# Kernel tuning notes

Measured on AMD Instinct MI355X. Metric: run time of the kernel, lower is better.

## Reference

```python
import jax, jax.numpy as jnp
import numpy as np

HID = 1024
NH = 16
HD = HID // NH  # 64


def _lin_params(key, fan_in, fan_out):
    k1, k2 = jax.random.split(key)
    lim = 1.0 / np.sqrt(fan_in)
    W = jax.random.uniform(k1, (fan_in, fan_out), jnp.float32, -lim, lim)
    b = jax.random.uniform(k2, (fan_out,), jnp.float32, -lim, lim)
    return W, b


def setup_inputs() -> dict:
    key = jax.random.key(0)
    ks = jax.random.split(key, 12)
    B, S = 4, 1024
    inp = {
        'query': jax.random.normal(ks[0], (B, S, HID), jnp.float32),
        'key': jax.random.normal(ks[1], (B, S, HID), jnp.float32),
        'value': jax.random.normal(ks[2], (B, S, HID), jnp.float32),
    }
    inp['Wq'], inp['bq'] = _lin_params(ks[3], HID, HID)
    inp['Wk'], inp['bk'] = _lin_params(ks[4], HID, HID)
    inp['Wv'], inp['bv'] = _lin_params(ks[5], HID, HID)
    inp['Wp'], inp['bp'] = _lin_params(ks[6], HID, HID)
    inp['Wup'], inp['bup'] = _lin_params(ks[7], HD, 1)
    inp['Wud'], inp['bud'] = _lin_params(ks[8], HD, 1)
    inp['Wus'], inp['bus'] = _lin_params(ks[9], HID, NH)
    inp['Wo'], inp['bo'] = _lin_params(ks[10], HID, HID)
    return inp


def _split_heads(x, B, S):
    # [B,S,HID] -> [B,NH,S,HD]
    return x.reshape(B, S, NH, HD).transpose(0, 2, 1, 3)


def reference(query, key, value, Wq, bq, Wk, bk, Wv, bv, Wp, bp,
              Wup, bup, Wud, bud, Wus, bus, Wo, bo):
    B, S, _ = query.shape
    len_q = S

    q = query @ Wq + bq   # [B,S,HID]
    k = key @ Wk + bk
    v = value @ Wv + bv

    # Gaussian-window positional bias (per head, per query position)
    p = _split_heads(q @ Wp + bp, B, S)              # [B,NH,S,HD]
    tp = jnp.tanh(p)
    p_i = tp @ Wup + bup                             # [B,NH,S,1]
    z_i = tp @ Wud + bud                             # [B,NH,S,1]
    cen_pos = len_q * jax.nn.sigmoid(p_i)            # [B,NH,S,1]
    win_size = len_q * jax.nn.sigmoid(z_i)           # [B,NH,S,1]
    pos = jnp.arange(len_q, dtype=q.dtype)[None, None, None, :]  # [1,1,1,S]
    bias = (pos - cen_pos) ** 2 / (0.5 * win_size ** 2)          # [B,NH,S,S]

    # per-head alpha gate from raw query
    alpha = jax.nn.sigmoid(query @ Wus + bus)        # [B,S,NH]
    alpha = alpha.reshape(B, S, NH, 1).transpose(0, 2, 1, 3)  # [B,NH,S,1]

    qh = _split_heads(q, B, S)
    kh = _split_heads(k, B, S)
    vh = _split_heads(v, B, S)

    scale = 1.0 / jnp.sqrt(jnp.asarray(HD, q.dtype))
    scores = jnp.einsum('bhqd,bhkd->bhqk', qh, kh) * scale
    scores = scores - alpha * bias                   # inject gated Gaussian bias
    attn = jax.nn.softmax(scores, axis=-1)           # [B,NH,S,S]

    out = jnp.einsum('bhqk,bhkd->bhqd', attn, vh)    # [B,NH,S,HD]
    x = out.transpose(0, 2, 1, 3).reshape(B, S, HID)
    x = x @ Wo + bo
    return x, attn
```

## Files before the change

### kernel.cpp

```cpp
#include <hip/hip_runtime.h>
#include <hip/hip_bf16.h>
#include <math.h>

#define S_LEN 1024
#define HIDN  1024
#define NHEAD 16
#define HDIM  64
#define BATCH 4
#define MTOT  (BATCH * S_LEN)

typedef __attribute__((ext_vector_type(8))) short          bf16v8;
typedef __attribute__((ext_vector_type(8))) unsigned short u16v8;
typedef __attribute__((ext_vector_type(4))) unsigned short u16v4;
typedef __attribute__((ext_vector_type(4))) float          f32v4;

__device__ __forceinline__ unsigned short f2bf_rne(float x) {
    unsigned int u = __float_as_uint(x);
    unsigned int r = (u + 0x7fffu + ((u >> 16) & 1u)) >> 16;
    return (unsigned short)r;
}
__device__ __forceinline__ float bf2f(unsigned short h) {
    return __uint_as_float(((unsigned int)h) << 16);
}
__device__ __forceinline__ void split2(float x, unsigned short& h, unsigned short& l) {
    h = f2bf_rne(x);
    l = f2bf_rne(x - bf2f(h));
}

__global__ __launch_bounds__(256) void split_a(
    const float* __restrict__ X, unsigned short* __restrict__ H,
    unsigned short* __restrict__ L)
{
    const int i = blockIdx.x * 256 + threadIdx.x;
    const float4 x0 = ((const float4*)X)[2 * i];
    const float4 x1 = ((const float4*)X)[2 * i + 1];
    float xs[8] = {x0.x, x0.y, x0.z, x0.w, x1.x, x1.y, x1.z, x1.w};
    u16v8 h, l;
#pragma unroll
    for (int j = 0; j < 8; ++j) {
        unsigned short hh, ll;
        split2(xs[j], hh, ll);
        h[j] = hh; l[j] = ll;
    }
    ((u16v8*)H)[i] = h;
    ((u16v8*)L)[i] = l;
}

__global__ __launch_bounds__(256) void split_w(
    const float* __restrict__ W, unsigned short* __restrict__ H,
    unsigned short* __restrict__ L)
{
    __shared__ float T[64][65];
    const int t  = threadIdx.x;
    const int k0 = blockIdx.y * 64;
    const int n0 = blockIdx.x * 64;

    const int r = t >> 4;
    const int c = (t & 15) * 4;
#pragma unroll
    for (int i = 0; i < 4; ++i) {
        const int rr = r + i * 16;
        const float4 v = *(const float4*)&W[(size_t)(k0 + rr) * 1024 + n0 + c];
        T[rr][c + 0] = v.x; T[rr][c + 1] = v.y;
        T[rr][c + 2] = v.z; T[rr][c + 3] = v.w;
    }
    __syncthreads();

    const int n  = t >> 2;
    const int ko = (t & 3) * 16;
    u16v8 h0, h1, l0, l1;
#pragma unroll
    for (int kk = 0; kk < 8; ++kk) {
        unsigned short hh, ll;
        split2(T[ko + kk][n], hh, ll);
        h0[kk] = hh; l0[kk] = ll;
    }
#pragma unroll
    for (int kk = 0; kk < 8; ++kk) {
        unsigned short hh, ll;
        split2(T[ko + 8 + kk][n], hh, ll);
        h1[kk] = hh; l1[kk] = ll;
    }
    unsigned short* Hp = &H[(size_t)(n0 + n) * 1024 + k0 + ko];
    unsigned short* Lp = &L[(size_t)(n0 + n) * 1024 + k0 + ko];
    *(u16v8*)(Hp)     = h0;
    *(u16v8*)(Hp + 8) = h1;
    *(u16v8*)(Lp)     = l0;
    *(u16v8*)(Lp + 8) = l1;
}

__global__ __launch_bounds__(256) void gemm_bf16x3(
    const unsigned short* __restrict__ Ah, const unsigned short* __restrict__ Al,
    const unsigned short* __restrict__ Bh, const unsigned short* __restrict__ Bl,
    const float* __restrict__ bias, float* __restrict__ Cf,
    unsigned short* __restrict__ Ch, unsigned short* __restrict__ Cl, int vt)
{
    __shared__ short Ash[128][40];
    __shared__ short Asl[128][40];
    __shared__ short Bsh[64][40];
    __shared__ short Bsl[64][40];

    const int t    = threadIdx.x;
    const int bm   = blockIdx.y * 128;
    const int bn   = blockIdx.x * 64;
    const int lane = t & 63;
    const int w    = t >> 6;
    const int wr   = w >> 1;
    const int wc   = w & 1;
    const int fr   = lane & 15;
    const int fq   = lane >> 4;
    const int ks   = fq * 8;

    f32v4 zero = {0.f, 0.f, 0.f, 0.f};
    f32v4 acc[4][2];
#pragma unroll
    for (int i = 0; i < 4; ++i)
#pragma unroll
        for (int j = 0; j < 2; ++j) acc[i][j] = zero;

    const int sr = t >> 2;
    const int sc = (t & 3) * 8;
    const unsigned short* pAh = &Ah[(size_t)(bm + sr) * 1024 + sc];
    const unsigned short* pAl = &Al[(size_t)(bm + sr) * 1024 + sc];
    const unsigned short* pBh = &Bh[(size_t)(bn + sr) * 1024 + sc];
    const unsigned short* pBl = &Bl[(size_t)(bn + sr) * 1024 + sc];
    const size_t arow2 = (size_t)64 * 1024;

    u16v8 rah0, rah1, ral0, ral1, rbh0, rbl0;
    auto LOAD = [&](int k0) {
        rah0 = *(const u16v8*)(pAh + k0);
        rah1 = *(const u16v8*)(pAh + arow2 + k0);
        ral0 = *(const u16v8*)(pAl + k0);
        ral1 = *(const u16v8*)(pAl + arow2 + k0);
        rbh0 = *(const u16v8*)(pBh + k0);
        rbl0 = *(const u16v8*)(pBl + k0);
    };

    LOAD(0);
    for (int k0 = 0; k0 < 1024; k0 += 32) {
        __syncthreads();
        *(u16v8*)&Ash[sr][sc]      = rah0;
        *(u16v8*)&Ash[sr + 64][sc] = rah1;
        *(u16v8*)&Asl[sr][sc]      = ral0;
        *(u16v8*)&Asl[sr + 64][sc] = ral1;
        *(u16v8*)&Bsh[sr][sc]      = rbh0;
        *(u16v8*)&Bsl[sr][sc]      = rbl0;
        __syncthreads();

        if (k0 + 32 < 1024) LOAD(k0 + 32);

        bf16v8 fah[4], fal[4], fbh[2], fbl[2];
#pragma unroll
        for (int i = 0; i < 4; ++i) {
            fah[i] = *(const bf16v8*)&Ash[wr * 64 + i * 16 + fr][ks];
            fal[i] = *(const bf16v8*)&Asl[wr * 64 + i * 16 + fr][ks];
        }
#pragma unroll
        for (int j = 0; j < 2; ++j) {
            fbh[j] = *(const bf16v8*)&Bsh[wc * 32 + j * 16 + fr][ks];
            fbl[j] = *(const bf16v8*)&Bsl[wc * 32 + j * 16 + fr][ks];
        }
#pragma unroll
        for (int i = 0; i < 4; ++i)
#pragma unroll
            for (int j = 0; j < 2; ++j) {
                acc[i][j] = __builtin_amdgcn_mfma_f32_16x16x32_bf16(
                    fah[i], fbh[j], acc[i][j], 0, 0, 0);
                acc[i][j] = __builtin_amdgcn_mfma_f32_16x16x32_bf16(
                    fah[i], fbl[j], acc[i][j], 0, 0, 0);
                acc[i][j] = __builtin_amdgcn_mfma_f32_16x16x32_bf16(
                    fal[i], fbh[j], acc[i][j], 0, 0, 0);
            }
    }

#pragma unroll
    for (int j = 0; j < 2; ++j) {
        const int col = bn + wc * 32 + j * 16 + fr;
        const float bb = bias[col];
#pragma unroll
        for (int i = 0; i < 4; ++i) {
            const int row0 = bm + wr * 64 + i * 16 + fq * 4;
            const f32v4 cv = acc[i][j];
            if (vt) {
                u16v4 h4, l4;
#pragma unroll
                for (int r = 0; r < 4; ++r) {
                    unsigned short hh, ll;
                    split2(cv[r] + bb, hh, ll);
                    h4[r] = hh; l4[r] = ll;
                }
                const size_t base =
                    ((size_t)((row0 >> 10) * 16 + (col >> 6)) * 64 + (col & 63)) * 1024
                    + (row0 & 1023);
                *(u16v4*)&Ch[base] = h4;
                *(u16v4*)&Cl[base] = l4;
            } else {
#pragma unroll
                for (int r = 0; r < 4; ++r) {
                    const float v = cv[r] + bb;
                    const size_t idx = (size_t)(row0 + r) * 1024 + col;
                    if (Cf) Cf[idx] = v;
                    if (Ch) {
                        unsigned short hh, ll;
                        split2(v, hh, ll);
                        Ch[idx] = hh; Cl[idx] = ll;
                    }
                }
            }
        }
    }
}

__global__ __launch_bounds__(256) void alpha_kernel(
    const float* __restrict__ X, const float* __restrict__ Wus,
    const float* __restrict__ bus, float* __restrict__ alpha)
{
    __shared__ float Ws[1024 * 16];
    const int t = threadIdx.x;
#pragma unroll
    for (int i = 0; i < 16; ++i) {
        const int idx = t + i * 256;
        *reinterpret_cast<float4*>(&Ws[idx * 4]) =
            *reinterpret_cast<const float4*>(&Wus[idx * 4]);
    }
    __syncthreads();

    const int r = t >> 4, c = t & 15;
    const size_t row = (size_t)blockIdx.x * 16 + r;
    const float* x = &X[row * 1024];
    float acc = 0.f;
    for (int kk = 0; kk < 1024; kk += 4) {
        const float4 xv = *reinterpret_cast<const float4*>(&x[kk]);
        acc = fmaf(xv.x, Ws[(kk + 0) * 16 + c], acc);
        acc = fmaf(xv.y, Ws[(kk + 1) * 16 + c], acc);
        acc = fmaf(xv.z, Ws[(kk + 2) * 16 + c], acc);
        acc = fmaf(xv.w, Ws[(kk + 3) * 16 + c], acc);
    }
    acc += bus[c];
    alpha[row * 16 + c] = 1.f / (1.f + expf(-acc));
}

__global__ __launch_bounds__(256) void posparam_kernel(
    const float* __restrict__ p, const float* __restrict__ alpha,
    const float* __restrict__ Wup, const float* __restrict__ bup,
    const float* __restrict__ Wud, const float* __restrict__ bud,
    float* __restrict__ cen, float* __restrict__ c0)
{
    __shared__ float wu[64], wd[64];
    const int t = threadIdx.x;
    if (t < 64) { wu[t] = Wup[t]; wd[t] = Wud[t]; }
    __syncthreads();

    const int tid = blockIdx.x * 256 + t;
    const int b = tid >> 14;
    const int h = (tid >> 10) & 15;
    const int s = tid & 1023;

    const float* pr = &p[((size_t)(b * 1024 + s)) * 1024 + h * 64];
    float ap = 0.f, az = 0.f;
#pragma unroll
    for (int d = 0; d < 64; d += 4) {
        const float4 pv = *reinterpret_cast<const float4*>(&pr[d]);
        const float t0 = tanhf(pv.x), t1 = tanhf(pv.y);
        const float t2 = tanhf(pv.z), t3 = tanhf(pv.w);
        ap += t0 * wu[d] + t1 * wu[d + 1] + t2 * wu[d + 2] + t3 * wu[d + 3];
        az += t0 * wd[d] + t1 * wd[d + 1] + t2 * wd[d + 2] + t3 * wd[d + 3];
    }
    ap += bup[0];
    az += bud[0];
    const float cenv = 1024.f / (1.f + expf(-ap));
    const float win  = 1024.f / (1.f + expf(-az));
    const float al   = alpha[(size_t)(b * 1024 + s) * 16 + h];
    const int oi = (b * 16 + h) * 1024 + s;
    cen[oi] = cenv;
    c0[oi]  = al * 2.f / (win * win);
}

#define M0_SHIFT 8.0f
__global__ __launch_bounds__(256, 3) void attn_fused(
    const unsigned short* __restrict__ qh, const unsigned short* __restrict__ ql,
    const unsigned short* __restrict__ kh, const unsigned short* __restrict__ kl,
    const unsigned short* __restrict__ vTh, const unsigned short* __restrict__ vTl,
    const float* __restrict__ cen, const float* __restrict__ c0,
    float* __restrict__ attn,
    unsigned short* __restrict__ oh, unsigned short* __restrict__ ol)
{
    __shared__ unsigned short KH[64][64], KL[64][64];
    __shared__ unsigned short VH[64][64], VL[64][64];
    __shared__ unsigned short PH[64][64], PL[64][64];
    __shared__ float CEN[64], C0S[64];
    __shared__ float LSUM[2][64];
    __shared__ float RINV[64];

    const int bid   = blockIdx.x;
    const int z     = ((bid >> 7) << 3) | (bid & 7);
    const int itile = (bid >> 3) & 15;
    const int i0    = itile * 64;
    const int bq    = z >> 4;
    const int hd    = z & 15;

    const int t    = threadIdx.x;
    const int lane = t & 63;
    const int w    = t >> 6;
    const int wr   = w >> 1, wc = w & 1;
    const int fr   = lane & 15, fq = lane >> 4;

    if (t < 64) {
        CEN[t] = cen[(size_t)z * 1024 + i0 + t];
        C0S[t] = c0[(size_t)z * 1024 + i0 + t];
    }

    bf16v8 qfh_[2][2], qfl_[2][2];
#pragma unroll
    for (int i = 0; i < 2; ++i)
#pragma unroll
        for (int kk = 0; kk < 2; ++kk) {
            const size_t qa = (size_t)(bq * 1024 + i0 + wr * 32 + i * 16 + fr) * 1024
                              + hd * 64 + kk * 32 + fq * 8;
            qfh_[i][kk] = *(const bf16v8*)&qh[qa];
            qfl_[i][kk] = *(const bf16v8*)&ql[qa];
        }

    float lsum[2][4];
#pragma unroll
    for (int i = 0; i < 2; ++i)
#pragma unroll
        for (int r = 0; r < 4; ++r) lsum[i][r] = 0.f;

    const f32v4 zero = {0.f, 0.f, 0.f, 0.f};

    for (int jt = 0; jt < 16; ++jt) {
        const int j0 = jt * 64;
        __syncthreads();
#pragma unroll
        for (int pp = 0; pp < 2; ++pp) {
            const int c   = t + pp * 256;
            const int row = c >> 3;
            const int seg = c & 7;
            const size_t ga = (size_t)(bq * 1024 + j0 + row) * 1024 + hd * 64 + seg * 8;
            const int sl = (seg ^ (row & 7)) * 8;
            *(u16v8*)&KH[row][sl] = *(const u16v8*)&kh[ga];
            *(u16v8*)&KL[row][sl] = *(const u16v8*)&kl[ga];
        }
        __syncthreads();

        f32v4 acc[2][2];
#pragma unroll
        for (int i = 0; i < 2; ++i)
#pragma unroll
            for (int j2 = 0; j2 < 2; ++j2) acc[i][j2] = zero;

#pragma unroll
        for (int kk = 0; kk < 2; ++kk) {
            bf16v8 fbh[2], fbl[2];
#pragma unroll
            for (int j2 = 0; j2 < 2; ++j2) {
                const int rb = wc * 32 + j2 * 16 + fr;
                const int sb = ((kk * 4 + fq) ^ (rb & 7)) * 8;
                fbh[j2] = *(const bf16v8*)&KH[rb][sb];
                fbl[j2] = *(const bf16v8*)&KL[rb][sb];
            }
#pragma unroll
            for (int i = 0; i < 2; ++i)
#pragma unroll
                for (int j2 = 0; j2 < 2; ++j2) {
                    acc[i][j2] = __builtin_amdgcn_mfma_f32_16x16x32_bf16(
                        qfh_[i][kk], fbh[j2], acc[i][j2], 0, 0, 0);
                    acc[i][j2] = __builtin_amdgcn_mfma_f32_16x16x32_bf16(
                        qfh_[i][kk], fbl[j2], acc[i][j2], 0, 0, 0);
                    acc[i][j2] = __builtin_amdgcn_mfma_f32_16x16x32_bf16(
                        qfl_[i][kk], fbh[j2], acc[i][j2], 0, 0, 0);
                }
        }

#pragma unroll
        for (int i = 0; i < 2; ++i)
#pragma unroll
            for (int r = 0; r < 4; ++r) {
                const int row = wr * 32 + i * 16 + fq * 4 + r;
                const float cv = CEN[row], cc = C0S[row];
                float al = 0.f;
#pragma unroll
                for (int j2 = 0; j2 < 2; ++j2) {
                    const int col = wc * 32 + j2 * 16 + fr;
                    const float dd = (float)(j0 + col) - cv;
                    const float s  = acc[i][j2][r] * 0.125f - cc * dd * dd;
                    al += __expf(s - M0_SHIFT);
                }
                lsum[i][r] += al;
            }
    }

#pragma unroll
    for (int i = 0; i < 2; ++i)
#pragma unroll
        for (int r = 0; r < 4; ++r) {
            float v = lsum[i][r];
            v += __shfl_xor(v, 1);
            v += __shfl_xor(v, 2);
            v += __shfl_xor(v, 4);
            v += __shfl_xor(v, 8);
            if (fr == 0) LSUM[wc][wr * 32 + i * 16 + fq * 4 + r] = v;
        }
    __syncthreads();
    if (t < 64) RINV[t] = 1.f / (LSUM[0][t] + LSUM[1][t]);

    f32v4 acco[2][2];
#pragma unroll
    for (int i = 0; i < 2; ++i)
#pragma unroll
        for (int j = 0; j < 2; ++j) acco[i][j] = zero;

    float* attnZ = attn + (size_t)z * 1024 * 1024;
    const unsigned short* vhb = vTh + (size_t)z * 64 * 1024;
    const unsigned short* vlb = vTl + (size_t)z * 64 * 1024;

    for (int jt = 0; jt < 16; ++jt) {
        const int j0 = jt * 64;
        __syncthreads();
#pragma unroll
        for (int pp = 0; pp < 2; ++pp) {
            const int c   = t + pp * 256;
            const int row = c >> 3;
            const int seg = c & 7;
            const size_t ga = (size_t)(bq * 1024 + j0 + row) * 1024 + hd * 64 + seg * 8;
            const int sl = (seg ^ (row & 7)) * 8;
            *(u16v8*)&KH[row][sl] = *(const u16v8*)&kh[ga];
            *(u16v8*)&KL[row][sl] = *(const u16v8*)&kl[ga];
            const size_t va = (size_t)row * 1024 + j0 + seg * 8;
            *(u16v8*)&VH[row][sl] = *(const u16v8*)&vhb[va];
            *(u16v8*)&VL[row][sl] = *(const u16v8*)&vlb[va];
        }
        __syncthreads();

        f32v4 acc[2][2];
#pragma unroll
        for (int i = 0; i < 2; ++i)
#pragma unroll
            for (int j2 = 0; j2 < 2; ++j2) acc[i][j2] = zero;

#pragma unroll
        for (int kk = 0; kk < 2; ++kk) {
            bf16v8 fbh[2], fbl[2];
#pragma unroll
            for (int j2 = 0; j2 < 2; ++j2) {
                const int rb = wc * 32 + j2 * 16 + fr;
                const int sb = ((kk * 4 + fq) ^ (rb & 7)) * 8;
                fbh[j2] = *(const bf16v8*)&KH[rb][sb];
                fbl[j2] = *(const bf16v8*)&KL[rb][sb];
            }
#pragma unroll
            for (int i = 0; i < 2; ++i)
#pragma unroll
                for (int j2 = 0; j2 < 2; ++j2) {
                    acc[i][j2] = __builtin_amdgcn_mfma_f32_16x16x32_bf16(
                        qfh_[i][kk], fbh[j2], acc[i][j2], 0, 0, 0);
                    acc[i][j2] = __builtin_amdgcn_mfma_f32_16x16x32_bf16(
                        qfh_[i][kk], fbl[j2], acc[i][j2], 0, 0, 0);
                    acc[i][j2] = __builtin_amdgcn_mfma_f32_16x16x32_bf16(
                        qfl_[i][kk], fbh[j2], acc[i][j2], 0, 0, 0);
                }
        }

#pragma unroll
        for (int i = 0; i < 2; ++i)
#pragma unroll
            for (int r = 0; r < 4; ++r) {
                const int row = wr * 32 + i * 16 + fq * 4 + r;
                const float cv = CEN[row], cc = C0S[row], ri = RINV[row];
#pragma unroll
                for (int j2 = 0; j2 < 2; ++j2) {
                    const int col = wc * 32 + j2 * 16 + fr;
                    const float dd = (float)(j0 + col) - cv;
                    const float s  = acc[i][j2][r] * 0.125f - cc * dd * dd;
                    const float p  = __expf(s - M0_SHIFT) * ri;
                    attnZ[(size_t)(i0 + row) * 1024 + j0 + col] = p;
                    unsigned short hv, lv;
                    split2(p, hv, lv);
                    const int slot = ((col >> 3) ^ (row & 7)) * 8 + (col & 7);
                    PH[row][slot] = hv;
                    PL[row][slot] = lv;
                }
            }
        __syncthreads();

#pragma unroll
        for (int kk = 0; kk < 2; ++kk) {
            bf16v8 pah[2], pal[2], fbh[2], fbl[2];
#pragma unroll
            for (int iq = 0; iq < 2; ++iq) {
                const int rp = wr * 32 + iq * 16 + fr;
                const int sp = ((kk * 4 + fq) ^ (rp & 7)) * 8;
                pah[iq] = *(const bf16v8*)&PH[rp][sp];
                pal[iq] = *(const bf16v8*)&PL[rp][sp];
            }
#pragma unroll
            for (int jd = 0; jd < 2; ++jd) {
                const int rb = wc * 32 + jd * 16 + fr;
                const int sb = ((kk * 4 + fq) ^ (rb & 7)) * 8;
                fbh[jd] = *(const bf16v8*)&VH[rb][sb];
                fbl[jd] = *(const bf16v8*)&VL[rb][sb];
            }
#pragma unroll
            for (int iq = 0; iq < 2; ++iq)
#pragma unroll
                for (int jd = 0; jd < 2; ++jd) {
                    acco[iq][jd] = __builtin_amdgcn_mfma_f32_16x16x32_bf16(
                        pah[iq], fbh[jd], acco[iq][jd], 0, 0, 0);
                    acco[iq][jd] = __builtin_amdgcn_mfma_f32_16x16x32_bf16(
                        pah[iq], fbl[jd], acco[iq][jd], 0, 0, 0);
                    acco[iq][jd] = __builtin_amdgcn_mfma_f32_16x16x32_bf16(
                        pal[iq], fbh[jd], acco[iq][jd], 0, 0, 0);
                }
        }
    }

#pragma unroll
    for (int jd = 0; jd < 2; ++jd) {
        const int dcol = wc * 32 + jd * 16 + fr;
#pragma unroll
        for (int iq = 0; iq < 2; ++iq) {
            const int row0 = i0 + wr * 32 + iq * 16 + fq * 4;
            const f32v4 cv = acco[iq][jd];
#pragma unroll
            for (int r = 0; r < 4; ++r) {
                unsigned short hv, lv;
                split2(cv[r], hv, lv);
                const size_t idx = (size_t)(bq * 1024 + row0 + r) * 1024 + hd * 64 + dcol;
                oh[idx] = hv;
                ol[idx] = lv;
            }
        }
    }
}

extern "C" void kernel_launch(void* const* d_in, const int* in_sizes, int n_in,
                              void* d_out, int out_size, void* d_ws, size_t ws_size,
                              hipStream_t stream)
{
    const float* query = (const float*)d_in[0];
    const float* key_  = (const float*)d_in[1];
    const float* value = (const float*)d_in[2];
    const float* Wq  = (const float*)d_in[3];
    const float* bq  = (const float*)d_in[4];
    const float* Wk  = (const float*)d_in[5];
    const float* bk  = (const float*)d_in[6];
    const float* Wv  = (const float*)d_in[7];
    const float* bv  = (const float*)d_in[8];
    const float* Wp  = (const float*)d_in[9];
    const float* bp  = (const float*)d_in[10];
    const float* Wup = (const float*)d_in[11];
    const float* bup = (const float*)d_in[12];
    const float* Wud = (const float*)d_in[13];
    const float* bud = (const float*)d_in[14];
    const float* Wus = (const float*)d_in[15];
    const float* bus = (const float*)d_in[16];
    const float* Wo  = (const float*)d_in[17];
    const float* bo  = (const float*)d_in[18];

    float* x_out = (float*)d_out;
    float* attn  = x_out + (size_t)MTOT * HIDN;

    char* wsb = (char*)d_ws;
    unsigned short* qh  = (unsigned short*)(wsb);
    unsigned short* ql  = (unsigned short*)(wsb + (8u  << 20));
    unsigned short* kh  = (unsigned short*)(wsb + (16u << 20));
    unsigned short* kl  = (unsigned short*)(wsb + (24u << 20));
    unsigned short* vTh = (unsigned short*)(wsb + (32u << 20));
    unsigned short* vTl = (unsigned short*)(wsb + (40u << 20));
    float* p_ws  = (float*)(wsb + (48u << 20));
    unsigned short* oh = (unsigned short*)(wsb + (48u << 20));
    unsigned short* ol = (unsigned short*)(wsb + (56u << 20));
    float* alpha_ws = (float*)(wsb + (64u << 20));
    float* cen_ws   = (float*)(wsb + (64u << 20) + (256u << 10));
    float* c0_ws    = (float*)(wsb + (64u << 20) + (512u << 10));
    unsigned short* ah = (unsigned short*)attn;
    unsigned short* al = ah + (size_t)MTOT * HIDN;
    unsigned short* wh = al + (size_t)MTOT * HIDN;
    unsigned short* wl = wh + (size_t)HIDN * HIDN;
    unsigned short* w2h = qh;
    unsigned short* w2l = ql;

    const dim3 blk(256);
    const dim3 gsplit_a(MTOT * HIDN / 8 / 256);
    const dim3 gsplit_w(16, 16);
    const dim3 ggemm(HIDN / 64, MTOT / 128);

    split_w<<<gsplit_w, blk, 0, stream>>>(Wq, wh, wl);
    split_a<<<gsplit_a, blk, 0, stream>>>(query, ah, al);
    gemm_bf16x3<<<ggemm, blk, 0, stream>>>(ah, al, wh, wl, bq, nullptr, qh, ql, 0);
    split_w<<<gsplit_w, blk, 0, stream>>>(Wk, wh, wl);
    split_a<<<gsplit_a, blk, 0, stream>>>(key_, ah, al);
    gemm_bf16x3<<<ggemm, blk, 0, stream>>>(ah, al, wh, wl, bk, nullptr, kh, kl, 0);
    split_w<<<gsplit_w, blk, 0, stream>>>(Wv, wh, wl);
    split_a<<<gsplit_a, blk, 0, stream>>>(value, ah, al);
    gemm_bf16x3<<<ggemm, blk, 0, stream>>>(ah, al, wh, wl, bv, nullptr, vTh, vTl, 1);
    split_w<<<gsplit_w, blk, 0, stream>>>(Wp, wh, wl);
    gemm_bf16x3<<<ggemm, blk, 0, stream>>>(qh, ql, wh, wl, bp, p_ws, nullptr, nullptr, 0);
    alpha_kernel<<<dim3(MTOT / 16), blk, 0, stream>>>(query, Wus, bus, alpha_ws);
    posparam_kernel<<<dim3((BATCH * NHEAD * S_LEN) / 256), blk, 0, stream>>>(
        p_ws, alpha_ws, Wup, bup, Wud, bud, cen_ws, c0_ws);
    attn_fused<<<dim3(1024), blk, 0, stream>>>(
        qh, ql, kh, kl, vTh, vTl, cen_ws, c0_ws, attn, oh, ol);
    split_w<<<gsplit_w, blk, 0, stream>>>(Wo, w2h, w2l);
    gemm_bf16x3<<<ggemm, blk, 0, stream>>>(oh, ol, w2h, w2l, bo, x_out,
                                           nullptr, nullptr, 0);
}
```

Before: 455.5 us.

## Double block size to 512 threads in GEMM and attention with register prefetch

The bf16x3 GEMM now runs 8 waves per 128x64 tile, with each wave owning a 32x32 sub-tile, and the global-to-LDS copy is spread over more threads. The fused attention kernel processes 128 query rows per block with 8 waves, so each K/V tile loaded into shared memory is reused across twice as many rows. K and V tiles are also prefetched into registers one iteration ahead to overlap the global loads with MFMA work. The cost is fewer blocks in the grid, more shared memory for P, and more register pressure under the new launch bounds.

```diff
diff --git a/kernel.cpp b/kernel.cpp
--- a/kernel.cpp
+++ b/kernel.cpp
@@ -89,7 +89,7 @@
     *(u16v8*)(Lp + 8) = l1;
 }
 
-__global__ __launch_bounds__(256) void gemm_bf16x3(
+__global__ __launch_bounds__(512, 4) void gemm_bf16x3(
     const unsigned short* __restrict__ Ah, const unsigned short* __restrict__ Al,
     const unsigned short* __restrict__ Bh, const unsigned short* __restrict__ Bl,
     const float* __restrict__ bias, float* __restrict__ Cf,
@@ -104,56 +104,54 @@
     const int bm   = blockIdx.y * 128;
     const int bn   = blockIdx.x * 64;
     const int lane = t & 63;
-    const int w    = t >> 6;
-    const int wr   = w >> 1;
-    const int wc   = w & 1;
+    const int wid  = t >> 6;
+    const int wr   = wid >> 1;
+    const int wc   = wid & 1;
     const int fr   = lane & 15;
     const int fq   = lane >> 4;
     const int ks   = fq * 8;
 
     f32v4 zero = {0.f, 0.f, 0.f, 0.f};
-    f32v4 acc[4][2];
-#pragma unroll
-    for (int i = 0; i < 4; ++i)
+    f32v4 acc[2][2];
+#pragma unroll
+    for (int i = 0; i < 2; ++i)
 #pragma unroll
         for (int j = 0; j < 2; ++j) acc[i][j] = zero;
 
-    const int sr = t >> 2;
-    const int sc = (t & 3) * 8;
-    const unsigned short* pAh = &Ah[(size_t)(bm + sr) * 1024 + sc];
-    const unsigned short* pAl = &Al[(size_t)(bm + sr) * 1024 + sc];
-    const unsigned short* pBh = &Bh[(size_t)(bn + sr) * 1024 + sc];
-    const unsigned short* pBl = &Bl[(size_t)(bn + sr) * 1024 + sc];
-    const size_t arow2 = (size_t)64 * 1024;
-
-    u16v8 rah0, rah1, ral0, ral1, rbh0, rbl0;
+    const int sra = t >> 2;
+    const int sca = (t & 3) * 8;
+    const int tb  = t & 255;
+    const int srb = tb >> 2;
+    const int scb = (tb & 3) * 8;
+    const bool isBl = (t >= 256);
+    const unsigned short* pAh = &Ah[(size_t)(bm + sra) * 1024 + sca];
+    const unsigned short* pAl = &Al[(size_t)(bm + sra) * 1024 + sca];
+    const unsigned short* pB  = isBl ? &Bl[(size_t)(bn + srb) * 1024 + scb]
+                                     : &Bh[(size_t)(bn + srb) * 1024 + scb];
+
+    u16v8 rah, ral, rb;
     auto LOAD = [&](int k0) {
-        rah0 = *(const u16v8*)(pAh + k0);
-        rah1 = *(const u16v8*)(pAh + arow2 + k0);
-        ral0 = *(const u16v8*)(pAl + k0);
-        ral1 = *(const u16v8*)(pAl + arow2 + k0);
-        rbh0 = *(const u16v8*)(pBh + k0);
-        rbl0 = *(const u16v8*)(pBl + k0);
+        rah = *(const u16v8*)(pAh + k0);
+        ral = *(const u16v8*)(pAl + k0);
+        rb  = *(const u16v8*)(pB  + k0);
     };
 
     LOAD(0);
     for (int k0 = 0; k0 < 1024; k0 += 32) {
         __syncthreads();
-        *(u16v8*)&Ash[sr][sc]      = rah0;
-        *(u16v8*)&Ash[sr + 64][sc] = rah1;
-        *(u16v8*)&Asl[sr][sc]      = ral0;
-        *(u16v8*)&Asl[sr + 64][sc] = ral1;
-        *(u16v8*)&Bsh[sr][sc]      = rbh0;
-        *(u16v8*)&Bsl[sr][sc]      = rbl0;
+        *(u16v8*)&Ash[sra][sca] = rah;
+        *(u16v8*)&Asl[sra][sca] = ral;
+        if (isBl) *(u16v8*)&Bsl[srb][scb] = rb;
+        else      *(u16v8*)&Bsh[srb][scb] = rb;
         __syncthreads();
 
         if (k0 + 32 < 1024) LOAD(k0 + 32);
 
-        bf16v8 fah[4], fal[4], fbh[2], fbl[2];
-#pragma unroll
-        for (int i = 0; i < 4; ++i) {
-            fah[i] = *(const bf16v8*)&Ash[wr * 64 + i * 16 + fr][ks];
-            fal[i] = *(const bf16v8*)&Asl[wr * 64 + i * 16 + fr][ks];
+        bf16v8 fah[2], fal[2], fbh[2], fbl[2];
+#pragma unroll
+        for (int i = 0; i < 2; ++i) {
+            fah[i] = *(const bf16v8*)&Ash[wr * 32 + i * 16 + fr][ks];
+            fal[i] = *(const bf16v8*)&Asl[wr * 32 + i * 16 + fr][ks];
         }
 #pragma unroll
         for (int j = 0; j < 2; ++j) {
@@ -161,7 +159,7 @@
             fbl[j] = *(const bf16v8*)&Bsl[wc * 32 + j * 16 + fr][ks];
         }
 #pragma unroll
-        for (int i = 0; i < 4; ++i)
+        for (int i = 0; i < 2; ++i)
 #pragma unroll
             for (int j = 0; j < 2; ++j) {
                 acc[i][j] = __builtin_amdgcn_mfma_f32_16x16x32_bf16(
@@ -178,8 +176,8 @@
         const int col = bn + wc * 32 + j * 16 + fr;
         const float bb = bias[col];
 #pragma unroll
-        for (int i = 0; i < 4; ++i) {
-            const int row0 = bm + wr * 64 + i * 16 + fq * 4;
+        for (int i = 0; i < 2; ++i) {
+            const int row0 = bm + wr * 32 + i * 16 + fq * 4;
             const f32v4 cv = acc[i][j];
             if (vt) {
                 u16v4 h4, l4;
@@ -277,7 +275,7 @@
 }
 
 #define M0_SHIFT 8.0f
-__global__ __launch_bounds__(256, 3) void attn_fused(
+__global__ __launch_bounds__(512, 4) void attn_fused(
     const unsigned short* __restrict__ qh, const unsigned short* __restrict__ ql,
     const unsigned short* __restrict__ kh, const unsigned short* __restrict__ kl,
     const unsigned short* __restrict__ vTh, const unsigned short* __restrict__ vTl,
@@ -287,25 +285,26 @@
 {
     __shared__ unsigned short KH[64][64], KL[64][64];
     __shared__ unsigned short VH[64][64], VL[64][64];
-    __shared__ unsigned short PH[64][64], PL[64][64];
-    __shared__ float CEN[64], C0S[64];
-    __shared__ float LSUM[2][64];
-    __shared__ float RINV[64];
+    __shared__ unsigned short PH[128][64], PL[128][64];
+    __shared__ float CEN[128], C0S[128];
+    __shared__ float LSUM[2][128];
+    __shared__ float RINV[128];
 
     const int bid   = blockIdx.x;
-    const int z     = ((bid >> 7) << 3) | (bid & 7);
-    const int itile = (bid >> 3) & 15;
-    const int i0    = itile * 64;
+    const int z     = ((bid >> 6) << 3) | (bid & 7);
+    const int itile = (bid >> 3) & 7;
+    const int i0    = itile * 128;
     const int bq    = z >> 4;
     const int hd    = z & 15;
 
     const int t    = threadIdx.x;
     const int lane = t & 63;
-    const int w    = t >> 6;
-    const int wr   = w >> 1, wc = w & 1;
+    const int wid  = t >> 6;
+    const int wrp  = wid >> 1;
+    const int wc   = wid & 1;
     const int fr   = lane & 15, fq = lane >> 4;
 
-    if (t < 64) {
+    if (t < 128) {
         CEN[t] = cen[(size_t)z * 1024 + i0 + t];
         C0S[t] = c0[(size_t)z * 1024 + i0 + t];
     }
@@ -315,7 +314,7 @@
     for (int i = 0; i < 2; ++i)
 #pragma unroll
         for (int kk = 0; kk < 2; ++kk) {
-            const size_t qa = (size_t)(bq * 1024 + i0 + wr * 32 + i * 16 + fr) * 1024
+            const size_t qa = (size_t)(bq * 1024 + i0 + wrp * 32 + i * 16 + fr) * 1024
                               + hd * 64 + kk * 32 + fq * 8;
             qfh_[i][kk] = *(const bf16v8*)&qh[qa];
             qfl_[i][kk] = *(const bf16v8*)&ql[qa];
@@ -329,20 +328,32 @@
 
     const f32v4 zero = {0.f, 0.f, 0.f, 0.f};
 
+    const int srow = t >> 3;
+    const int sseg = t & 7;
+    const int ssl  = (sseg ^ (srow & 7)) * 8;
+    const unsigned short* vhb = vTh + (size_t)z * 64 * 1024;
+    const unsigned short* vlb = vTl + (size_t)z * 64 * 1024;
+
+    u16v8 rkh, rkl, rvh, rvl;
+    auto LOADK = [&](int j0) {
+        const size_t ga = (size_t)(bq * 1024 + j0 + srow) * 1024 + hd * 64 + sseg * 8;
+        rkh = *(const u16v8*)&kh[ga];
+        rkl = *(const u16v8*)&kl[ga];
+    };
+    auto LOADV = [&](int j0) {
+        const size_t va = (size_t)srow * 1024 + j0 + sseg * 8;
+        rvh = *(const u16v8*)&vhb[va];
+        rvl = *(const u16v8*)&vlb[va];
+    };
+
+    LOADK(0);
     for (int jt = 0; jt < 16; ++jt) {
         const int j0 = jt * 64;
         __syncthreads();
-#pragma unroll
-        for (int pp = 0; pp < 2; ++pp) {
-            const int c   = t + pp * 256;
-            const int row = c >> 3;
-            const int seg = c & 7;
-            const size_t ga = (size_t)(bq * 1024 + j0 + row) * 1024 + hd * 64 + seg * 8;
-            const int sl = (seg ^ (row & 7)) * 8;
-            *(u16v8*)&KH[row][sl] = *(const u16v8*)&kh[ga];
-            *(u16v8*)&KL[row][sl] = *(const u16v8*)&kl[ga];
-        }
+        *(u16v8*)&KH[srow][ssl] = rkh;
+        *(u16v8*)&KL[srow][ssl] = rkl;
         __syncthreads();
+        if (jt < 15) LOADK(j0 + 64);
 
         f32v4 acc[2][2];
 #pragma unroll
@@ -377,7 +388,7 @@
         for (int i = 0; i < 2; ++i)
 #pragma unroll
             for (int r = 0; r < 4; ++r) {
-                const int row = wr * 32 + i * 16 + fq * 4 + r;
+                const int row = wrp * 32 + i * 16 + fq * 4 + r;
                 const float cv = CEN[row], cc = C0S[row];
                 float al = 0.f;
 #pragma unroll
@@ -400,10 +411,10 @@
             v += __shfl_xor(v, 2);
             v += __shfl_xor(v, 4);
             v += __shfl_xor(v, 8);
-            if (fr == 0) LSUM[wc][wr * 32 + i * 16 + fq * 4 + r] = v;
+            if (fr == 0) LSUM[wc][wrp * 32 + i * 16 + fq * 4 + r] = v;
         }
     __syncthreads();
-    if (t < 64) RINV[t] = 1.f / (LSUM[0][t] + LSUM[1][t]);
+    if (t < 128) RINV[t] = 1.f / (LSUM[0][t] + LSUM[1][t]);
 
     f32v4 acco[2][2];
 #pragma unroll
@@ -412,26 +423,18 @@
         for (int j = 0; j < 2; ++j) acco[i][j] = zero;
 
     float* attnZ = attn + (size_t)z * 1024 * 1024;
-    const unsigned short* vhb = vTh + (size_t)z * 64 * 1024;
-    const unsigned short* vlb = vTl + (size_t)z * 64 * 1024;
-
+
+    LOADK(0);
+    LOADV(0);
     for (int jt = 0; jt < 16; ++jt) {
         const int j0 = jt * 64;
         __syncthreads();
-#pragma unroll
-        for (int pp = 0; pp < 2; ++pp) {
-            const int c   = t + pp * 256;
-            const int row = c >> 3;
-            const int seg = c & 7;
-            const size_t ga = (size_t)(bq * 1024 + j0 + row) * 1024 + hd * 64 + seg * 8;
-            const int sl = (seg ^ (row & 7)) * 8;
-            *(u16v8*)&KH[row][sl] = *(const u16v8*)&kh[ga];
-            *(u16v8*)&KL[row][sl] = *(const u16v8*)&kl[ga];
-            const size_t va = (size_t)row * 1024 + j0 + seg * 8;
-            *(u16v8*)&VH[row][sl] = *(const u16v8*)&vhb[va];
-            *(u16v8*)&VL[row][sl] = *(const u16v8*)&vlb[va];
-        }
+        *(u16v8*)&KH[srow][ssl] = rkh;
+        *(u16v8*)&KL[srow][ssl] = rkl;
+        *(u16v8*)&VH[srow][ssl] = rvh;
+        *(u16v8*)&VL[srow][ssl] = rvl;
         __syncthreads();
+        if (jt < 15) { LOADK(j0 + 64); LOADV(j0 + 64); }
 
         f32v4 acc[2][2];
 #pragma unroll
@@ -466,7 +469,7 @@
         for (int i = 0; i < 2; ++i)
 #pragma unroll
             for (int r = 0; r < 4; ++r) {
-                const int row = wr * 32 + i * 16 + fq * 4 + r;
+                const int row = wrp * 32 + i * 16 + fq * 4 + r;
                 const float cv = CEN[row], cc = C0S[row], ri = RINV[row];
 #pragma unroll
                 for (int j2 = 0; j2 < 2; ++j2) {
@@ -489,7 +492,7 @@
             bf16v8 pah[2], pal[2], fbh[2], fbl[2];
 #pragma unroll
             for (int iq = 0; iq < 2; ++iq) {
-                const int rp = wr * 32 + iq * 16 + fr;
+                const int rp = wrp * 32 + iq * 16 + fr;
                 const int sp = ((kk * 4 + fq) ^ (rp & 7)) * 8;
                 pah[iq] = *(const bf16v8*)&PH[rp][sp];
                 pal[iq] = *(const bf16v8*)&PL[rp][sp];
@@ -520,7 +523,7 @@
         const int dcol = wc * 32 + jd * 16 + fr;
 #pragma unroll
         for (int iq = 0; iq < 2; ++iq) {
-            const int row0 = i0 + wr * 32 + iq * 16 + fq * 4;
+            const int row0 = i0 + wrp * 32 + iq * 16 + fq * 4;
             const f32v4 cv = acco[iq][jd];
 #pragma unroll
             for (int r = 0; r < 4; ++r) {
@@ -582,27 +585,28 @@
     unsigned short* w2l = ql;
 
     const dim3 blk(256);
+    const dim3 blk512(512);
     const dim3 gsplit_a(MTOT * HIDN / 8 / 256);
     const dim3 gsplit_w(16, 16);
     const dim3 ggemm(HIDN / 64, MTOT / 128);
 
     split_w<<<gsplit_w, blk, 0, stream>>>(Wq, wh, wl);
     split_a<<<gsplit_a, blk, 0, stream>>>(query, ah, al);
-    gemm_bf16x3<<<ggemm, blk, 0, stream>>>(ah, al, wh, wl, bq, nullptr, qh, ql, 0);
+    gemm_bf16x3<<<ggemm, blk512, 0, stream>>>(ah, al, wh, wl, bq, nullptr, qh, ql, 0);
     split_w<<<gsplit_w, blk, 0, stream>>>(Wk, wh, wl);
     split_a<<<gsplit_a, blk, 0, stream>>>(key_, ah, al);
-    gemm_bf16x3<<<ggemm, blk, 0, stream>>>(ah, al, wh, wl, bk, nullptr, kh, kl, 0);
+    gemm_bf16x3<<<ggemm, blk512, 0, stream>>>(ah, al, wh, wl, bk, nullptr, kh, kl, 0);
     split_w<<<gsplit_w, blk, 0, stream>>>(Wv, wh, wl);
     split_a<<<gsplit_a, blk, 0, stream>>>(value, ah, al);
-    gemm_bf16x3<<<ggemm, blk, 0, stream>>>(ah, al, wh, wl, bv, nullptr, vTh, vTl, 1);
+    gemm_bf16x3<<<ggemm, blk512, 0, stream>>>(ah, al, wh, wl, bv, nullptr, vTh, vTl, 1);
     split_w<<<gsplit_w, blk, 0, stream>>>(Wp, wh, wl);
-    gemm_bf16x3<<<ggemm, blk, 0, stream>>>(qh, ql, wh, wl, bp, p_ws, nullptr, nullptr, 0);
+    gemm_bf16x3<<<ggemm, blk512, 0, stream>>>(qh, ql, wh, wl, bp, p_ws, nullptr, nullptr, 0);
     alpha_kernel<<<dim3(MTOT / 16), blk, 0, stream>>>(query, Wus, bus, alpha_ws);
     posparam_kernel<<<dim3((BATCH * NHEAD * S_LEN) / 256), blk, 0, stream>>>(
         p_ws, alpha_ws, Wup, bup, Wud, bud, cen_ws, c0_ws);
-    attn_fused<<<dim3(1024), blk, 0, stream>>>(
+    attn_fused<<<dim3(512), blk512, 0, stream>>>(
         qh, ql, kh, kl, vTh, vTl, cen_ws, c0_ws, attn, oh, ol);
     split_w<<<gsplit_w, blk, 0, stream>>>(Wo, w2h, w2l);
-    gemm_bf16x3<<<ggemm, blk, 0, stream>>>(oh, ol, w2h, w2l, bo, x_out,
-                                           nullptr, nullptr, 0);
-}
+    gemm_bf16x3<<<ggemm, blk512, 0, stream>>>(oh, ol, w2h, w2l, bo, x_out,
+                                              nullptr, nullptr, 0);
+}
```

Measured after the change: 506.1 us. +11.1%, slower.
